# Optimization experiments

Measured on AMD Instinct MI355X. Metric: run time of the kernel, lower is better.

Reference implementation:

```python
import math
import jax, jax.numpy as jnp
import numpy as np

H = 16  # n_heads


def setup_inputs() -> dict:
    key = jax.random.key(0)
    ks = jax.random.split(key, 12)
    b, n, dm = 4, 1024, 1024
    s = 1.0 / math.sqrt(dm)
    inp = {
        'query': jax.random.normal(ks[0], (b, n, dm), jnp.float32),
        'key':   jax.random.normal(ks[1], (b, n, dm), jnp.float32),
        'value': jax.random.normal(ks[2], (b, n, dm), jnp.float32),
        'Wq': jax.random.normal(ks[3], (dm, dm), jnp.float32) * s,
        'bq': jnp.zeros((dm,), jnp.float32),
        'Wk': jax.random.normal(ks[4], (dm, dm), jnp.float32) * s,
        'bk': jnp.zeros((dm,), jnp.float32),
        'Wv': jax.random.normal(ks[5], (dm, dm), jnp.float32) * s,
        'bv': jnp.zeros((dm,), jnp.float32),
        'Wo': jax.random.normal(ks[6], (dm, dm), jnp.float32) * s,
        'bo': jnp.zeros((dm,), jnp.float32),
    }
    return inp


def reference(query, key, value, Wq, bq, Wk, bk, Wv, bv, Wo, bo):
    b, n, dm = query.shape
    dk = dm // H

    def proj(x, W, bias):
        # Linear(d_model,d_model) then split heads: [b,n,dm] -> [b,h,n,dk]
        y = x @ W.T + bias
        return y.reshape(b, n, H, dk).transpose(0, 2, 1, 3)

    q = proj(query, Wq, bq)
    k = proj(key, Wk, bk)
    v = proj(value, Wv, bv)

    scores = jnp.einsum('bhid,bhjd->bhij', q, k) / math.sqrt(dk)  # [b,h,n,n]
    p_attn = jax.nn.softmax(scores, axis=-1)
    # softmax(ones) along last dim is exactly uniform 1/n
    p_ident = jnp.full_like(scores, 1.0 / n)
    rnd = jax.random.normal(jax.random.key(42), scores.shape, scores.dtype)
    p_rand = jax.nn.softmax(rnd, axis=-1)

    # FAITHFUL to source: einsum('b h i j, b h i d -> b h i d', p, value)
    # i.e. value scaled by row-sum of the attention probs (== value up to numerics)
    def weight(p):
        return v * jnp.sum(p, axis=-1, keepdims=True)  # [b,h,n,dk]

    x = weight(p_attn)
    y = weight(p_ident)
    z = weight(p_rand)

    def merge(t):  # [b,h,n,dk] -> [b,n,dm]
        return t.transpose(0, 2, 1, 3).reshape(b, n, dm)

    return (merge(x) @ Wo.T + bo, merge(y), merge(z))
```

## Files before the change

kernel.cpp:

```cpp
#include <hip/hip_runtime.h>
#include <hip/hip_bf16.h>
#include <stdint.h>

using bf16 = __hip_bfloat16;
typedef __attribute__((ext_vector_type(8))) __bf16 bf16x8;
typedef __attribute__((ext_vector_type(4))) float f32x4;

__global__ __launch_bounds__(256) void cast4_kernel(const float* __restrict__ in,
                                                    bf16* __restrict__ out) {
    const size_t i = ((size_t)blockIdx.x * 256 + threadIdx.x) * 4;
    const float4 v = *(const float4*)(in + i);
    bf16 h0 = __float2bfloat16(v.x), h1 = __float2bfloat16(v.y);
    bf16 h2 = __float2bfloat16(v.z), h3 = __float2bfloat16(v.w);
    uint2 u;
    u.x = (uint32_t)(*(const uint16_t*)&h0) | ((uint32_t)(*(const uint16_t*)&h1) << 16);
    u.y = (uint32_t)(*(const uint16_t*)&h2) | ((uint32_t)(*(const uint16_t*)&h3) << 16);
    *(uint2*)(out + i) = u;
}

#define TM 128
#define TN 128
#define BK 32

__global__ __launch_bounds__(256) void gemm_bt(
    const bf16* __restrict__ A, const bf16* __restrict__ B,
    const float* __restrict__ bias,
    float* __restrict__ C0, float* __restrict__ C1, bf16* __restrict__ Cb,
    int M, int N, int K)
{
    __shared__ bf16 As[TM * BK];
    __shared__ bf16 Bs[TN * BK];

    const int tid  = threadIdx.x;
    const int lane = tid & 63;
    const int wave = tid >> 6;
    const int wm   = (wave >> 1) * 64;
    const int wn   = (wave & 1) * 64;

    const int bm = blockIdx.x * TM;
    const int bn = blockIdx.y * TN;

    f32x4 acc[4][4] = {};

    const int c0 = wave * 128 + lane;
    const int c1 = c0 + 64;
    const bf16* gA0 = A + (size_t)(bm + (c0 >> 2)) * K + (c0 & 3) * 8;
    const bf16* gA1 = A + (size_t)(bm + (c1 >> 2)) * K + (c1 & 3) * 8;
    const bf16* gB0 = B + (size_t)(bn + (c0 >> 2)) * K + (c0 & 3) * 8;
    const bf16* gB1 = B + (size_t)(bn + (c1 >> 2)) * K + (c1 & 3) * 8;
    bf16* lA0 = As + (size_t)(wave * 128) * 8;
    bf16* lA1 = lA0 + 64 * 8;
    bf16* lB0 = Bs + (size_t)(wave * 128) * 8;
    bf16* lB1 = lB0 + 64 * 8;

    const int fr = lane & 15;
    const int fk = (lane >> 4) * 8;

    for (int k0 = 0; k0 < K; k0 += BK) {
        __builtin_amdgcn_global_load_lds(
            (const __attribute__((address_space(1))) void*)(gA0 + k0),
            (__attribute__((address_space(3))) void*)lA0, 16, 0, 0);
        __builtin_amdgcn_global_load_lds(
            (const __attribute__((address_space(1))) void*)(gA1 + k0),
            (__attribute__((address_space(3))) void*)lA1, 16, 0, 0);
        __builtin_amdgcn_global_load_lds(
            (const __attribute__((address_space(1))) void*)(gB0 + k0),
            (__attribute__((address_space(3))) void*)lB0, 16, 0, 0);
        __builtin_amdgcn_global_load_lds(
            (const __attribute__((address_space(1))) void*)(gB1 + k0),
            (__attribute__((address_space(3))) void*)lB1, 16, 0, 0);
        __syncthreads();

        bf16x8 af[4], bg[4];
        #pragma unroll
        for (int t = 0; t < 4; ++t) {
            af[t] = *(const bf16x8*)(As + (wm + t * 16 + fr) * BK + fk);
            bg[t] = *(const bf16x8*)(Bs + (wn + t * 16 + fr) * BK + fk);
        }
        #pragma unroll
        for (int i = 0; i < 4; ++i)
            #pragma unroll
            for (int j = 0; j < 4; ++j)
                acc[i][j] = __builtin_amdgcn_mfma_f32_16x16x32_bf16(
                    af[i], bg[j], acc[i][j], 0, 0, 0);
        __syncthreads();
    }

    const int quad = lane >> 4;
    #pragma unroll
    for (int j = 0; j < 4; ++j) {
        const int col = bn + wn + j * 16 + fr;
        const float bb = bias ? bias[col] : 0.0f;
        #pragma unroll
        for (int i = 0; i < 4; ++i) {
            const int row0 = bm + wm + i * 16 + quad * 4;
            #pragma unroll
            for (int r = 0; r < 4; ++r) {
                const float v = acc[i][j][r] + bb;
                const size_t idx = (size_t)(row0 + r) * N + col;
                C0[idx] = v;
                if (C1) C1[idx] = v;
                if (Cb) Cb[idx] = __float2bfloat16(v);
            }
        }
    }
}

__global__ __launch_bounds__(256) void gemm_f32_naive(
    const float* __restrict__ A, const float* __restrict__ B,
    const float* __restrict__ bias,
    float* __restrict__ C0, float* __restrict__ C1,
    int M, int N, int K)
{
    const size_t idx = (size_t)blockIdx.x * 256 + threadIdx.x;
    if (idx >= (size_t)M * N) return;
    const int row = (int)(idx / N), col = (int)(idx % N);
    const float* a = A + (size_t)row * K;
    const float* b = B + (size_t)col * K;
    float s = bias ? bias[col] : 0.0f;
    for (int k = 0; k < K; ++k) s += a[k] * b[k];
    C0[idx] = s;
    if (C1) C1[idx] = s;
}

extern "C" void kernel_launch(void* const* d_in, const int* in_sizes, int n_in,
                              void* d_out, int out_size, void* d_ws, size_t ws_size,
                              hipStream_t stream)
{
    const float* value = (const float*)d_in[2];
    const float* Wv    = (const float*)d_in[7];
    const float* bv    = (const float*)d_in[8];
    const float* Wo    = (const float*)d_in[9];
    const float* bo    = (const float*)d_in[10];

    const int dm = in_sizes[8];
    const int M  = in_sizes[2] / dm;
    const size_t MN = (size_t)M * dm;

    float* out0 = (float*)d_out;
    float* out1 = out0 + MN;
    float* out2 = out1 + MN;

    const size_t need = MN * 2 + (size_t)dm * dm * 4 + MN * 2;
    if (ws_size >= need && (M % TM) == 0 && (dm % TN) == 0 && (dm % BK) == 0) {
        char* ws = (char*)d_ws;
        bf16* value_b = (bf16*)ws;
        bf16* Wv_b    = (bf16*)(ws + MN * 2);
        bf16* Wo_b    = (bf16*)(ws + MN * 2 + (size_t)dm * dm * 2);
        bf16* V_b     = (bf16*)(ws + MN * 2 + (size_t)dm * dm * 4);

        cast4_kernel<<<(int)(MN / 1024), 256, 0, stream>>>(value, value_b);
        cast4_kernel<<<dm * dm / 1024, 256, 0, stream>>>(Wv, Wv_b);
        cast4_kernel<<<dm * dm / 1024, 256, 0, stream>>>(Wo, Wo_b);

        dim3 grid(M / TM, dm / TN);
        gemm_bt<<<grid, 256, 0, stream>>>(value_b, Wv_b, bv, out1, out2, V_b, M, dm, dm);
        gemm_bt<<<grid, 256, 0, stream>>>(V_b, Wo_b, bo, out0, nullptr, nullptr, M, dm, dm);
    } else {
        const int nblk = (int)((MN + 255) / 256);
        gemm_f32_naive<<<nblk, 256, 0, stream>>>(value, Wv, bv, out1, out2, M, dm, dm);
        gemm_f32_naive<<<nblk, 256, 0, stream>>>(out1, Wo, bo, out0, nullptr, M, dm, dm);
    }
}
```

Measured before the change: 178.1 us.

## Fold Wo into Wv as combined weight and run both projections in one GEMM

Precomputes Wc = Wo·Wv and a combined bias bc = Wo·bv + bo, so the output projection can be computed directly from value alongside the V projection in a single GEMM over a concatenated weight [Wv; Wc]. The three cast kernels are merged into one prep kernel that also transposes Wv and reduces the bias. This removes the serial dependency between the two large GEMMs and the bf16 intermediate V write and read, at the cost of a small dm×dm GEMM per call. The layout assumes Wv_b and Wc_b are contiguous in the workspace so that Wv_b can serve as Bcat. Composing the weights in bf16 also changes the numerics of out0.

```diff
diff --git a/kernel.cpp b/kernel.cpp
--- a/kernel.cpp
+++ b/kernel.cpp
@@ -6,37 +6,152 @@
 typedef __attribute__((ext_vector_type(8))) __bf16 bf16x8;
 typedef __attribute__((ext_vector_type(4))) float f32x4;
 
-__global__ __launch_bounds__(256) void cast4_kernel(const float* __restrict__ in,
-                                                    bf16* __restrict__ out) {
-    const size_t i = ((size_t)blockIdx.x * 256 + threadIdx.x) * 4;
-    const float4 v = *(const float4*)(in + i);
-    bf16 h0 = __float2bfloat16(v.x), h1 = __float2bfloat16(v.y);
-    bf16 h2 = __float2bfloat16(v.z), h3 = __float2bfloat16(v.w);
-    uint2 u;
-    u.x = (uint32_t)(*(const uint16_t*)&h0) | ((uint32_t)(*(const uint16_t*)&h1) << 16);
-    u.y = (uint32_t)(*(const uint16_t*)&h2) | ((uint32_t)(*(const uint16_t*)&h3) << 16);
-    *(uint2*)(out + i) = u;
+static __device__ __forceinline__ bf16 f2b(float x) { return __float2bfloat16(x); }
+
+__global__ __launch_bounds__(256) void prep_kernel(
+    const float* __restrict__ value, const float* __restrict__ Wv,
+    const float* __restrict__ Wo, const float* __restrict__ bv,
+    const float* __restrict__ bo,
+    bf16* __restrict__ value_b, bf16* __restrict__ Wv_b,
+    bf16* __restrict__ Wo_b, bf16* __restrict__ WvT_b,
+    float* __restrict__ bc,
+    int nbVal, int nbW, int nbT, int dm)
+{
+    const int b = blockIdx.x;
+    const int tid = threadIdx.x;
+
+    if (b < nbVal) {
+        const size_t i = ((size_t)b * 256 + tid) * 4;
+        const float4 v = *(const float4*)(value + i);
+        bf16 h0 = f2b(v.x), h1 = f2b(v.y), h2 = f2b(v.z), h3 = f2b(v.w);
+        uint2 u;
+        u.x = (uint32_t)(*(const uint16_t*)&h0) | ((uint32_t)(*(const uint16_t*)&h1) << 16);
+        u.y = (uint32_t)(*(const uint16_t*)&h2) | ((uint32_t)(*(const uint16_t*)&h3) << 16);
+        *(uint2*)(value_b + i) = u;
+    } else if (b < nbVal + nbW) {
+        const size_t i = ((size_t)(b - nbVal) * 256 + tid) * 4;
+        const float4 v = *(const float4*)(Wo + i);
+        bf16 h0 = f2b(v.x), h1 = f2b(v.y), h2 = f2b(v.z), h3 = f2b(v.w);
+        uint2 u;
+        u.x = (uint32_t)(*(const uint16_t*)&h0) | ((uint32_t)(*(const uint16_t*)&h1) << 16);
+        u.y = (uint32_t)(*(const uint16_t*)&h2) | ((uint32_t)(*(const uint16_t*)&h3) << 16);
+        *(uint2*)(Wo_b + i) = u;
+    } else if (b < nbVal + nbW + nbT) {
+        __shared__ bf16 tile[32][33];
+        const int t = b - nbVal - nbW;
+        const int tpr = dm / 32;
+        const int i0 = (t / tpr) * 32, j0 = (t % tpr) * 32;
+        const int tx = tid & 31, ty = tid >> 5;
+        #pragma unroll
+        for (int p = 0; p < 4; ++p) {
+            const int r = ty + p * 8;
+            const float v = Wv[(size_t)(i0 + r) * dm + j0 + tx];
+            const bf16 h = f2b(v);
+            Wv_b[(size_t)(i0 + r) * dm + j0 + tx] = h;
+            tile[r][tx] = h;
+        }
+        __syncthreads();
+        #pragma unroll
+        for (int p = 0; p < 4; ++p) {
+            const int c = ty + p * 8;
+            WvT_b[(size_t)(j0 + c) * dm + i0 + tx] = tile[tx][c];
+        }
+    } else {
+        __shared__ float red[4];
+        const int row = b - nbVal - nbW - nbT;
+        const float* wrow = Wo + (size_t)row * dm;
+        float s = 0.f;
+        for (int k = tid; k < dm; k += 256) s += wrow[k] * bv[k];
+        #pragma unroll
+        for (int off = 32; off >= 1; off >>= 1) s += __shfl_down(s, off, 64);
+        if ((tid & 63) == 0) red[tid >> 6] = s;
+        __syncthreads();
+        if (tid == 0) bc[row] = red[0] + red[1] + red[2] + red[3] + bo[row];
+    }
+}
+
+__global__ __launch_bounds__(256) void gemm64_bt_b16out(
+    const bf16* __restrict__ A, const bf16* __restrict__ B,
+    bf16* __restrict__ C, int M, int N, int K)
+{
+    __shared__ bf16 As[64 * 32];
+    __shared__ bf16 Bs[64 * 32];
+
+    const int tid = threadIdx.x;
+    const int lane = tid & 63;
+    const int wave = tid >> 6;
+    const int wm = (wave >> 1) * 32;
+    const int wn = (wave & 1) * 32;
+    const int bm = blockIdx.x * 64;
+    const int bn = blockIdx.y * 64;
+
+    f32x4 acc[2][2] = {};
+
+    const int c = wave * 64 + lane;
+    const bf16* gA = A + (size_t)(bm + (c >> 2)) * K + (c & 3) * 8;
+    const bf16* gB = B + (size_t)(bn + (c >> 2)) * K + (c & 3) * 8;
+    bf16* lA = As + (size_t)c * 8;
+    bf16* lB = Bs + (size_t)c * 8;
+
+    const int fr = lane & 15;
+    const int fk = (lane >> 4) * 8;
+
+    for (int k0 = 0; k0 < K; k0 += 32) {
+        __builtin_amdgcn_global_load_lds(
+            (const __attribute__((address_space(1))) void*)(gA + k0),
+            (__attribute__((address_space(3))) void*)lA, 16, 0, 0);
+        __builtin_amdgcn_global_load_lds(
+            (const __attribute__((address_space(1))) void*)(gB + k0),
+            (__attribute__((address_space(3))) void*)lB, 16, 0, 0);
+        __syncthreads();
+        bf16x8 af[2], bg[2];
+        #pragma unroll
+        for (int t = 0; t < 2; ++t) {
+            af[t] = *(const bf16x8*)(As + (wm + t * 16 + fr) * 32 + fk);
+            bg[t] = *(const bf16x8*)(Bs + (wn + t * 16 + fr) * 32 + fk);
+        }
+        #pragma unroll
+        for (int i = 0; i < 2; ++i)
+            #pragma unroll
+            for (int j = 0; j < 2; ++j)
+                acc[i][j] = __builtin_amdgcn_mfma_f32_16x16x32_bf16(
+                    af[i], bg[j], acc[i][j], 0, 0, 0);
+        __syncthreads();
+    }
+
+    const int quad = lane >> 4;
+    #pragma unroll
+    for (int j = 0; j < 2; ++j) {
+        const int col = bn + wn + j * 16 + fr;
+        #pragma unroll
+        for (int i = 0; i < 2; ++i) {
+            const int row0 = bm + wm + i * 16 + quad * 4;
+            #pragma unroll
+            for (int r = 0; r < 4; ++r)
+                C[(size_t)(row0 + r) * N + col] = f2b(acc[i][j][r]);
+        }
+    }
 }
 
 #define TM 128
 #define TN 128
 #define BK 32
 
-__global__ __launch_bounds__(256) void gemm_bt(
-    const bf16* __restrict__ A, const bf16* __restrict__ B,
-    const float* __restrict__ bias,
-    float* __restrict__ C0, float* __restrict__ C1, bf16* __restrict__ Cb,
-    int M, int N, int K)
+__global__ __launch_bounds__(256) void gemm_fused(
+    const bf16* __restrict__ A, const bf16* __restrict__ Bcat,
+    const float* __restrict__ bv, const float* __restrict__ bc,
+    float* __restrict__ out0, float* __restrict__ out1, float* __restrict__ out2,
+    int M, int dm)
 {
     __shared__ bf16 As[TM * BK];
     __shared__ bf16 Bs[TN * BK];
 
-    const int tid  = threadIdx.x;
+    const int K = dm;
+    const int tid = threadIdx.x;
     const int lane = tid & 63;
     const int wave = tid >> 6;
-    const int wm   = (wave >> 1) * 64;
-    const int wn   = (wave & 1) * 64;
-
+    const int wm = (wave >> 1) * 64;
+    const int wn = (wave & 1) * 64;
     const int bm = blockIdx.x * TM;
     const int bn = blockIdx.y * TN;
 
@@ -46,8 +161,8 @@
     const int c1 = c0 + 64;
     const bf16* gA0 = A + (size_t)(bm + (c0 >> 2)) * K + (c0 & 3) * 8;
     const bf16* gA1 = A + (size_t)(bm + (c1 >> 2)) * K + (c1 & 3) * 8;
-    const bf16* gB0 = B + (size_t)(bn + (c0 >> 2)) * K + (c0 & 3) * 8;
-    const bf16* gB1 = B + (size_t)(bn + (c1 >> 2)) * K + (c1 & 3) * 8;
+    const bf16* gB0 = Bcat + (size_t)(bn + (c0 >> 2)) * K + (c0 & 3) * 8;
+    const bf16* gB1 = Bcat + (size_t)(bn + (c1 >> 2)) * K + (c1 & 3) * 8;
     bf16* lA0 = As + (size_t)(wave * 128) * 8;
     bf16* lA1 = lA0 + 64 * 8;
     bf16* lB0 = Bs + (size_t)(wave * 128) * 8;
@@ -86,21 +201,25 @@
         __syncthreads();
     }
 
+    const bool second = (bn >= dm);
+    const int cb = bn + wn - (second ? dm : 0);
+    const float* bias = second ? bc : bv;
+    float* o0 = second ? out0 : out1;
+    float* o1 = second ? nullptr : out2;
     const int quad = lane >> 4;
     #pragma unroll
     for (int j = 0; j < 4; ++j) {
-        const int col = bn + wn + j * 16 + fr;
-        const float bb = bias ? bias[col] : 0.0f;
+        const int col = cb + j * 16 + fr;
+        const float bb = bias[col];
         #pragma unroll
         for (int i = 0; i < 4; ++i) {
             const int row0 = bm + wm + i * 16 + quad * 4;
             #pragma unroll
             for (int r = 0; r < 4; ++r) {
                 const float v = acc[i][j][r] + bb;
-                const size_t idx = (size_t)(row0 + r) * N + col;
-                C0[idx] = v;
-                if (C1) C1[idx] = v;
-                if (Cb) Cb[idx] = __float2bfloat16(v);
+                const size_t idx = (size_t)(row0 + r) * dm + col;
+                o0[idx] = v;
+                if (o1) o1[idx] = v;
             }
         }
     }
@@ -141,21 +260,31 @@
     float* out1 = out0 + MN;
     float* out2 = out1 + MN;
 
-    const size_t need = MN * 2 + (size_t)dm * dm * 4 + MN * 2;
-    if (ws_size >= need && (M % TM) == 0 && (dm % TN) == 0 && (dm % BK) == 0) {
+    const size_t need = MN * 2 + (size_t)dm * dm * 2 * 4 + (size_t)dm * 4;
+    const bool ok = (ws_size >= need) && (M % TM == 0) && (dm % TM == 0) &&
+                    (dm % 32 == 0) && (MN % 1024 == 0);
+    if (ok) {
         char* ws = (char*)d_ws;
-        bf16* value_b = (bf16*)ws;
-        bf16* Wv_b    = (bf16*)(ws + MN * 2);
-        bf16* Wo_b    = (bf16*)(ws + MN * 2 + (size_t)dm * dm * 2);
-        bf16* V_b     = (bf16*)(ws + MN * 2 + (size_t)dm * dm * 4);
-
-        cast4_kernel<<<(int)(MN / 1024), 256, 0, stream>>>(value, value_b);
-        cast4_kernel<<<dm * dm / 1024, 256, 0, stream>>>(Wv, Wv_b);
-        cast4_kernel<<<dm * dm / 1024, 256, 0, stream>>>(Wo, Wo_b);
-
-        dim3 grid(M / TM, dm / TN);
-        gemm_bt<<<grid, 256, 0, stream>>>(value_b, Wv_b, bv, out1, out2, V_b, M, dm, dm);
-        gemm_bt<<<grid, 256, 0, stream>>>(V_b, Wo_b, bo, out0, nullptr, nullptr, M, dm, dm);
+        bf16* value_b = (bf16*)ws;                                   ws += MN * 2;
+        bf16* Wv_b    = (bf16*)ws;                                   ws += (size_t)dm * dm * 2;
+        bf16* Wc_b    = (bf16*)ws;                                   ws += (size_t)dm * dm * 2;
+        bf16* Wo_b    = (bf16*)ws;                                   ws += (size_t)dm * dm * 2;
+        bf16* WvT_b   = (bf16*)ws;                                   ws += (size_t)dm * dm * 2;
+        float* bc     = (float*)ws;
+
+        const int nbVal = (int)(MN / 1024);
+        const int nbW   = dm * dm / 1024;
+        const int nbT   = (dm / 32) * (dm / 32);
+        prep_kernel<<<nbVal + nbW + nbT + dm, 256, 0, stream>>>(
+            value, Wv, Wo, bv, bo, value_b, Wv_b, Wo_b, WvT_b, bc,
+            nbVal, nbW, nbT, dm);
+
+        dim3 g64(dm / 64, dm / 64);
+        gemm64_bt_b16out<<<g64, 256, 0, stream>>>(Wo_b, WvT_b, Wc_b, dm, dm, dm);
+
+        dim3 grid(M / TM, 2 * dm / TN);
+        gemm_fused<<<grid, 256, 0, stream>>>(value_b, Wv_b ,
+                                             bv, bc, out0, out1, out2, M, dm);
     } else {
         const int nblk = (int)((MN + 255) / 256);
         gemm_f32_naive<<<nblk, 256, 0, stream>>>(value, Wv, bv, out1, out2, M, dm, dm);
```

New measurement: 165.2 us. -7.2%, faster.
